# Kernel tuning notes

Hardware: AMD Instinct MI355X
Metric: run time of the kernel (lower is better)

The kernel has to match this reference:

```python
import jax, jax.numpy as jnp
import numpy as np

HEAD = 8


def setup_inputs() -> dict:
    key0 = jax.random.key(0)
    ks = jax.random.split(key0, 16)
    B, K, RD, NH = 16, 1024, 1024, 1024
    s = 0.02
    inp = {
        "v": jax.random.normal(ks[0], (B, K, RD), jnp.float32),
        "key": jax.random.normal(ks[1], (B, K, RD), jnp.float32),
        "query": jax.random.normal(ks[2], (B, K, RD), jnp.float32),
        "mask": jax.random.randint(ks[3], (B, 1, 1, K), 0, 2).astype(bool),
        # FCNet([relation_dim, num_hid], act='') == Linear(relation_dim, num_hid)
        "Wq": jax.random.normal(ks[4], (RD, NH), jnp.float32) * s,
        "bq": jnp.zeros((NH,), jnp.float32),
        "Wk": jax.random.normal(ks[5], (RD, NH), jnp.float32) * s,
        "bk": jnp.zeros((NH,), jnp.float32),
        "Wv": jax.random.normal(ks[6], (RD, NH), jnp.float32) * s,
        "bv": jnp.zeros((NH,), jnp.float32),
        "Wm": jax.random.normal(ks[7], (NH, NH), jnp.float32) * s,
        "bm": jnp.zeros((NH,), jnp.float32),
    }
    return inp


def reference(v, key, query, mask, Wq, bq, Wk, bk, Wv, bv, Wm, bm):
    B, K, _ = v.shape
    NH = Wq.shape[1]
    dk = NH // HEAD

    def split_heads(x):  # [B,K,NH] -> [B,H,K,dk]
        return x.reshape(B, K, HEAD, dk).transpose(0, 2, 1, 3)

    q = split_heads(query @ Wq + bq)
    k = split_heads(key @ Wk + bk)
    vv = split_heads(v @ Wv + bv)

    scores = jnp.einsum("bhqd,bhkd->bhqk", q, k) / jnp.sqrt(jnp.float32(dk))
    scores = jnp.where(mask, jnp.float32(-1e9), scores)
    att = jax.nn.softmax(scores, axis=-1)  # dropout is identity at eval
    atted = jnp.einsum("bhqk,bhkd->bhqd", att, vv)
    atted = atted.transpose(0, 2, 1, 3).reshape(B, K, NH)
    atted = atted @ Wm + bm
    return atted, att
```

## Files before the change

kernel.cpp:

```cpp
#include <hip/hip_runtime.h>

typedef unsigned short u16;
typedef __attribute__((ext_vector_type(8))) short short8;
typedef __attribute__((ext_vector_type(4))) float floatx4;

#define MFMA16(a, b, c) __builtin_amdgcn_mfma_f32_16x16x32_bf16(a, b, c, 0, 0, 0)

#define BB 16
#define KK 1024
#define NH 1024
#define HD 8
#define DK 128
#define ATT_OFF 16777216

typedef const __attribute__((address_space(1))) unsigned gl_u32;
typedef __attribute__((address_space(3))) unsigned lds_u32;

__device__ __forceinline__ u16 f2bf(float x) {
  unsigned u = __builtin_bit_cast(unsigned, x);
  u += 0x7fffu + ((u >> 16) & 1u);
  return (u16)(u >> 16);
}

__device__ __forceinline__ void gload16(const u16* g, u16* l) {
  __builtin_amdgcn_global_load_lds((gl_u32*)g, (lds_u32*)l, 16, 0, 0);
}

__global__ __launch_bounds__(256) void cast3_bf16x8(
    const float* __restrict__ i0, const float* __restrict__ i1,
    const float* __restrict__ i2, u16* __restrict__ o0, u16* __restrict__ o1,
    u16* __restrict__ o2) {
  const float* in = blockIdx.y == 0 ? i0 : (blockIdx.y == 1 ? i1 : i2);
  u16* out = blockIdx.y == 0 ? o0 : (blockIdx.y == 1 ? o1 : o2);
  const size_t i = ((size_t)blockIdx.x * 256 + threadIdx.x) * 8;
  float4 f0 = *(const float4*)(in + i);
  float4 f1 = *(const float4*)(in + i + 4);
  union { u16 u[8]; uint4 v; } p;
  p.u[0] = f2bf(f0.x); p.u[1] = f2bf(f0.y); p.u[2] = f2bf(f0.z); p.u[3] = f2bf(f0.w);
  p.u[4] = f2bf(f1.x); p.u[5] = f2bf(f1.y); p.u[6] = f2bf(f1.z); p.u[7] = f2bf(f1.w);
  *(uint4*)(out + i) = p.v;
}

__global__ __launch_bounds__(256) void tr_w4(
    const float* __restrict__ w0, const float* __restrict__ w1,
    const float* __restrict__ w2, const float* __restrict__ w3,
    u16* __restrict__ o0, u16* __restrict__ o1, u16* __restrict__ o2,
    u16* __restrict__ o3) {
  const int z = blockIdx.z;
  const float* in = z == 0 ? w0 : (z == 1 ? w1 : (z == 2 ? w2 : w3));
  u16* out = z == 0 ? o0 : (z == 1 ? o1 : (z == 2 ? o2 : o3));
  __shared__ u16 t[32][36];
  const int tid = threadIdx.x;
  const int bx = blockIdx.x * 32;
  const int by = blockIdx.y * 32;
  const int r = tid >> 3, c4 = (tid & 7) * 4;
  float4 f = *(const float4*)(in + (size_t)(by + r) * 1024 + bx + c4);
  t[r][c4 + 0] = f2bf(f.x);
  t[r][c4 + 1] = f2bf(f.y);
  t[r][c4 + 2] = f2bf(f.z);
  t[r][c4 + 3] = f2bf(f.w);
  __syncthreads();
  union { u16 u[4]; uint2 v; } p;
#pragma unroll
  for (int i = 0; i < 4; i++) p.u[i] = t[c4 + i][r];
  *(uint2*)(out + (size_t)(bx + r) * 1024 + by + c4) = p.v;
}

__global__ __launch_bounds__(256) void tr_head(const u16* __restrict__ vvb,
                                               u16* __restrict__ vvT) {
  __shared__ u16 t[32][36];
  const int tid = threadIdx.x;
  const int bh = blockIdx.z, b = bh >> 3, h = bh & 7;
  const int i0 = blockIdx.x * 32, d0 = blockIdx.y * 32;
  const int r = tid >> 3, c4 = (tid & 7) * 4;
  union { u16 u[4]; uint2 v; } p;
  p.v = *(const uint2*)(vvb + (size_t)(b * KK + i0 + r) * NH + h * DK + d0 + c4);
  t[r][c4 + 0] = p.u[0];
  t[r][c4 + 1] = p.u[1];
  t[r][c4 + 2] = p.u[2];
  t[r][c4 + 3] = p.u[3];
  __syncthreads();
#pragma unroll
  for (int i = 0; i < 4; i++) p.u[i] = t[c4 + i][r];
  *(uint2*)(vvT + (size_t)(bh * DK + d0 + r) * KK + i0 + c4) = p.v;
}

__device__ __forceinline__ void gemm_body(
    const u16* __restrict__ Ab, const u16* __restrict__ Bb,
    const float* __restrict__ bias, u16* __restrict__ Cb, float* __restrict__ Cf,
    const int Kd, const int ldc, const int nBase, const int mBase) {
  __shared__ __align__(16) u16 As[2][128 * 32];
  __shared__ __align__(16) u16 Bs[2][128 * 32];
  const int tid = threadIdx.x;
  const int wid = tid >> 6, lane = tid & 63;
  const int wm = (wid & 1) * 64, wn = (wid >> 1) * 64;
  const int lm = lane & 15, lq = lane >> 4;
  const int rIn = lane >> 2;
  const int sSlot = (lane & 3) * 8;

  const u16* aS0 = Ab + (size_t)(mBase + (wid * 2 + 0) * 16 + rIn) * Kd + sSlot;
  const u16* aS1 = Ab + (size_t)(mBase + (wid * 2 + 1) * 16 + rIn) * Kd + sSlot;
  const u16* bS0 = Bb + (size_t)(nBase + (wid * 2 + 0) * 16 + rIn) * Kd + sSlot;
  const u16* bS1 = Bb + (size_t)(nBase + (wid * 2 + 1) * 16 + rIn) * Kd + sSlot;

  floatx4 acc[4][4] = {};

  gload16(aS0, &As[0][(wid * 2 + 0) * 512]);
  gload16(aS1, &As[0][(wid * 2 + 1) * 512]);
  gload16(bS0, &Bs[0][(wid * 2 + 0) * 512]);
  gload16(bS1, &Bs[0][(wid * 2 + 1) * 512]);
  __syncthreads();

  int cur = 0;
  for (int k0 = 0; k0 < Kd; k0 += 32) {
    const int nxt = cur ^ 1;
    if (k0 + 32 < Kd) {
      gload16(aS0 + k0 + 32, &As[nxt][(wid * 2 + 0) * 512]);
      gload16(aS1 + k0 + 32, &As[nxt][(wid * 2 + 1) * 512]);
      gload16(bS0 + k0 + 32, &Bs[nxt][(wid * 2 + 0) * 512]);
      gload16(bS1 + k0 + 32, &Bs[nxt][(wid * 2 + 1) * 512]);
    }
    short8 af[4], bfr[4];
#pragma unroll
    for (int t = 0; t < 4; t++) {
      af[t]  = *(const short8*)&As[cur][(wm + t * 16 + lm) * 32 + lq * 8];
      bfr[t] = *(const short8*)&Bs[cur][(wn + t * 16 + lm) * 32 + lq * 8];
    }
#pragma unroll
    for (int i = 0; i < 4; i++)
#pragma unroll
      for (int j = 0; j < 4; j++)
        acc[i][j] = MFMA16(af[i], bfr[j], acc[i][j]);
    __syncthreads();
    cur = nxt;
  }

#pragma unroll
  for (int i = 0; i < 4; i++) {
    const int rowL = wm + i * 16 + lq * 4;
#pragma unroll
    for (int j = 0; j < 4; j++) {
      const int col = nBase + wn + j * 16 + lm;
      const float bval = bias ? bias[col] : 0.0f;
      const size_t base = (size_t)(mBase + rowL) * ldc + col;
#pragma unroll
      for (int r = 0; r < 4; r++) {
        const float v = acc[i][j][r] + bval;
        if (Cb) Cb[base + (size_t)r * ldc] = f2bf(v);
        if (Cf) Cf[base + (size_t)r * ldc] = v;
      }
    }
  }
}

__device__ __forceinline__ int2 swz_grid() {
  const int flat = blockIdx.x + 8 * blockIdx.y;
  const int xcd = flat & 7, idx = flat >> 3;
  const int nflat = xcd * 128 + idx;
  return make_int2((nflat & 7) * 128, (nflat >> 3) * 128);
}

__global__ __launch_bounds__(256, 2) void gemm_bt(
    const u16* __restrict__ A, const u16* __restrict__ Bt,
    const float* __restrict__ bias, u16* __restrict__ Cb, float* __restrict__ Cf) {
  int2 nm = swz_grid();
  gemm_body(A, Bt, bias, Cb, Cf, 1024, 1024, nm.x, nm.y);
}

__global__ __launch_bounds__(256, 2) void gemm_qkv(
    const u16* __restrict__ A0, const u16* __restrict__ A1,
    const u16* __restrict__ A2, const u16* __restrict__ B0,
    const u16* __restrict__ B1, const u16* __restrict__ B2,
    const float* __restrict__ b0, const float* __restrict__ b1,
    const float* __restrict__ b2, u16* __restrict__ C0, u16* __restrict__ C1,
    u16* __restrict__ C2) {
  const int z = blockIdx.z;
  const u16* A = z == 0 ? A0 : (z == 1 ? A1 : A2);
  const u16* B = z == 0 ? B0 : (z == 1 ? B1 : B2);
  const float* bias = z == 0 ? b0 : (z == 1 ? b1 : b2);
  u16* C = z == 0 ? C0 : (z == 1 ? C1 : C2);
  int2 nm = swz_grid();
  gemm_body(A, B, bias, C, nullptr, 1024, 1024, nm.x, nm.y);
}

__global__ __launch_bounds__(256, 2) void scores_softmax_pv(
    const u16* __restrict__ qb, const u16* __restrict__ kb,
    const int* __restrict__ mask, const u16* __restrict__ vvT,
    float* __restrict__ att, u16* __restrict__ atp) {
  __shared__ __align__(16) u16 p_lds[32 * 1024];
  u16* msk16 = p_lds;
  float* redM = (float*)&p_lds[1024];
  float* redS = (float*)&p_lds[1280];
  const int tid = threadIdx.x;

  const int flat = blockIdx.x + 32 * blockIdx.y;
  const int xcd = flat & 7, idx = flat >> 3;
  const int bh = xcd * 16 + (idx >> 5);
  const int rowBlk = idx & 31;

  const int b = bh >> 3, h = bh & 7;
  const int wid = tid >> 6, lane = tid & 63;
  const int lm = lane & 15, lq = lane >> 4;
  const int rowG = rowBlk * 32;

  {
    int4 m = *(const int4*)(mask + (size_t)b * KK + tid * 4);
    msk16[tid * 4 + 0] = (u16)(m.x != 0);
    msk16[tid * 4 + 1] = (u16)(m.y != 0);
    msk16[tid * 4 + 2] = (u16)(m.z != 0);
    msk16[tid * 4 + 3] = (u16)(m.w != 0);
  }

  short8 qf[2][4];
#pragma unroll
  for (int g = 0; g < 2; g++) {
    const u16* qp = qb + (size_t)(b * KK + rowG + g * 16 + lm) * NH + h * DK + lq * 8;
#pragma unroll
    for (int ks = 0; ks < 4; ks++) qf[g][ks] = *(const short8*)(qp + ks * 32);
  }

  floatx4 acc[2][16] = {};
  const u16* kpB = kb + (size_t)(b * KK + wid * 256 + lm) * NH + h * DK + lq * 8;
#pragma unroll
  for (int jt = 0; jt < 16; jt++) {
    const u16* kp = kpB + (size_t)jt * 16 * NH;
    short8 k0 = *(const short8*)(kp + 0);
    short8 k1 = *(const short8*)(kp + 32);
    short8 k2 = *(const short8*)(kp + 64);
    short8 k3 = *(const short8*)(kp + 96);
    floatx4 a0 = acc[0][jt], a1 = acc[1][jt];
    a0 = MFMA16(qf[0][0], k0, a0);
    a1 = MFMA16(qf[1][0], k0, a1);
    a0 = MFMA16(qf[0][1], k1, a0);
    a1 = MFMA16(qf[1][1], k1, a1);
    a0 = MFMA16(qf[0][2], k2, a0);
    a1 = MFMA16(qf[1][2], k2, a1);
    a0 = MFMA16(qf[0][3], k3, a0);
    a1 = MFMA16(qf[1][3], k3, a1);
    acc[0][jt] = a0;
    acc[1][jt] = a1;
  }
  __syncthreads();

  const float scale = 0.08838834764831845f;
  float mrow[2][4];
#pragma unroll
  for (int g = 0; g < 2; g++)
#pragma unroll
    for (int r = 0; r < 4; r++) mrow[g][r] = -3e38f;
#pragma unroll
  for (int jt = 0; jt < 16; jt++) {
    const int col = wid * 256 + jt * 16 + lm;
    const bool mk = msk16[col] != 0;
#pragma unroll
    for (int g = 0; g < 2; g++)
#pragma unroll
      for (int r = 0; r < 4; r++) {
        float s = mk ? -1e9f : acc[g][jt][r] * scale;
        acc[g][jt][r] = s;
        mrow[g][r] = fmaxf(mrow[g][r], s);
      }
  }
#pragma unroll
  for (int off = 1; off < 16; off <<= 1)
#pragma unroll
    for (int g = 0; g < 2; g++)
#pragma unroll
      for (int r = 0; r < 4; r++)
        mrow[g][r] = fmaxf(mrow[g][r], __shfl_xor(mrow[g][r], off));
  if (lm == 0) {
#pragma unroll
    for (int g = 0; g < 2; g++)
#pragma unroll
      for (int r = 0; r < 4; r++)
        redM[wid * 32 + g * 16 + lq * 4 + r] = mrow[g][r];
  }
  __syncthreads();
#pragma unroll
  for (int g = 0; g < 2; g++)
#pragma unroll
    for (int r = 0; r < 4; r++) {
      const int e = g * 16 + lq * 4 + r;
      mrow[g][r] = fmaxf(fmaxf(redM[0 + e], redM[32 + e]),
                         fmaxf(redM[64 + e], redM[96 + e]));
    }

  float srow[2][4] = {};
#pragma unroll
  for (int jt = 0; jt < 16; jt++)
#pragma unroll
    for (int g = 0; g < 2; g++)
#pragma unroll
      for (int r = 0; r < 4; r++) {
        float e = __expf(acc[g][jt][r] - mrow[g][r]);
        acc[g][jt][r] = e;
        srow[g][r] += e;
      }
#pragma unroll
  for (int off = 1; off < 16; off <<= 1)
#pragma unroll
    for (int g = 0; g < 2; g++)
#pragma unroll
      for (int r = 0; r < 4; r++) srow[g][r] += __shfl_xor(srow[g][r], off);
  if (lm == 0) {
#pragma unroll
    for (int g = 0; g < 2; g++)
#pragma unroll
      for (int r = 0; r < 4; r++)
        redS[wid * 32 + g * 16 + lq * 4 + r] = srow[g][r];
  }
  __syncthreads();
#pragma unroll
  for (int g = 0; g < 2; g++)
#pragma unroll
    for (int r = 0; r < 4; r++) {
      const int e = g * 16 + lq * 4 + r;
      srow[g][r] = 1.0f / (redS[0 + e] + redS[32 + e] + redS[64 + e] + redS[96 + e]);
    }
  __syncthreads();

#pragma unroll
  for (int g = 0; g < 2; g++)
#pragma unroll
    for (int r = 0; r < 4; r++) {
      const int row = g * 16 + lq * 4 + r;
#pragma unroll
      for (int jt = 0; jt < 16; jt++) {
        const int col = wid * 256 + jt * 16 + lm;
        const float p = acc[g][jt][r] * srow[g][r];
        acc[g][jt][r] = p;
        p_lds[(row * 1024 + col) ^ ((row & 7) << 3)] = f2bf(p);
      }
    }
  __syncthreads();

  floatx4 pacc[2][2] = {};
  const u16* vBase = vvT + (size_t)bh * DK * KK + (size_t)(wid * 32 + lm) * KK + lq * 8;
#pragma unroll 8
  for (int s = 0; s < 32; s++) {
    short8 v0 = *(const short8*)(vBase + s * 32);
    short8 v1 = *(const short8*)(vBase + 16 * KK + s * 32);
    short8 pf0 = *(const short8*)&p_lds[((0 + lm) * 1024 + s * 32 + lq * 8) ^ ((lm & 7) << 3)];
    short8 pf1 = *(const short8*)&p_lds[((16 + lm) * 1024 + s * 32 + lq * 8) ^ ((lm & 7) << 3)];
    pacc[0][0] = MFMA16(pf0, v0, pacc[0][0]);
    pacc[0][1] = MFMA16(pf0, v1, pacc[0][1]);
    pacc[1][0] = MFMA16(pf1, v0, pacc[1][0]);
    pacc[1][1] = MFMA16(pf1, v1, pacc[1][1]);
  }

#pragma unroll
  for (int g = 0; g < 2; g++)
#pragma unroll
    for (int r = 0; r < 4; r++) {
      const int row = rowG + g * 16 + lq * 4 + r;
      atp[(size_t)(b * KK + row) * NH + h * DK + wid * 32 + 0 + lm] = f2bf(pacc[g][0][r]);
      atp[(size_t)(b * KK + row) * NH + h * DK + wid * 32 + 16 + lm] = f2bf(pacc[g][1][r]);
    }

#pragma unroll
  for (int g = 0; g < 2; g++)
#pragma unroll
    for (int r = 0; r < 4; r++) {
      const int row = g * 16 + lq * 4 + r;
      float* attRow = att + ((size_t)bh * KK + rowG + row) * KK;
#pragma unroll
      for (int jt = 0; jt < 16; jt++) {
        const int col = wid * 256 + jt * 16 + lm;
        __builtin_nontemporal_store(acc[g][jt][r], attRow + col);
      }
    }
}

extern "C" void kernel_launch(void* const* d_in, const int* in_sizes, int n_in,
                              void* d_out, int out_size, void* d_ws, size_t ws_size,
                              hipStream_t stream) {
  const float* v     = (const float*)d_in[0];
  const float* key   = (const float*)d_in[1];
  const float* query = (const float*)d_in[2];
  const int*   mask  = (const int*)d_in[3];
  const float* Wq = (const float*)d_in[4];
  const float* bq = (const float*)d_in[5];
  const float* Wk = (const float*)d_in[6];
  const float* bk = (const float*)d_in[7];
  const float* Wv = (const float*)d_in[8];
  const float* bv = (const float*)d_in[9];
  const float* Wm = (const float*)d_in[10];
  const float* bm = (const float*)d_in[11];

  float* atted = (float*)d_out;
  float* att   = atted + (size_t)ATT_OFF;

  char* ws = (char*)d_ws;
  u16* qb   = (u16*)(ws + 0);
  u16* kb   = (u16*)(ws + 33554432ll);
  u16* vvb  = (u16*)(ws + 67108864ll);
  u16* vvT  = (u16*)(ws + 100663296ll);
  u16* atp  = (u16*)(ws + 134217728ll);
  u16* WqT  = (u16*)(ws + 167772160ll);
  u16* WkT  = (u16*)(ws + 169869312ll);
  u16* WvT  = (u16*)(ws + 171966464ll);
  u16* WmT  = (u16*)(ws + 174063616ll);

  u16* cq = (u16*)att;
  u16* ck = cq + 16777216;
  u16* cv = ck + 16777216;

  cast3_bf16x8<<<dim3(8192, 3), 256, 0, stream>>>(query, key, v, cq, ck, cv);

  tr_w4<<<dim3(32, 32, 4), 256, 0, stream>>>(Wq, Wk, Wv, Wm, WqT, WkT, WvT, WmT);

  gemm_qkv<<<dim3(8, 128, 3), 256, 0, stream>>>(cq, ck, cv, WqT, WkT, WvT,
                                                bq, bk, bv, qb, kb, vvb);

  tr_head<<<dim3(32, 4, 128), 256, 0, stream>>>(vvb, vvT);

  scores_softmax_pv<<<dim3(32, 128), 256, 0, stream>>>(qb, kb, mask, vvT, att, atp);

  gemm_bt<<<dim3(8, 128), 256, 0, stream>>>(atp, WmT, bm, nullptr, atted);
}
```

Before: 1.122 ms.

## Split attention block across eight waves and add MFMA priority hints

The fused scores/softmax/PV kernel now runs with 512 threads per block, so each wave owns 128 key columns instead of 256 and half the accumulator registers. The aim is more resident waves to hide latency on the K and V loads and the large att stores. The cross-wave max and sum reductions now combine eight partials. The PV loop splits its accumulation across two interleaved accumulators, and s_setprio hints are placed around the MFMA groups. In exchange, each wave re-reads the full Q fragment and the softmax reductions do more work.

```diff
diff --git a/kernel.cpp b/kernel.cpp
--- a/kernel.cpp
+++ b/kernel.cpp
@@ -183,14 +183,14 @@
   gemm_body(A, B, bias, C, nullptr, 1024, 1024, nm.x, nm.y);
 }
 
-__global__ __launch_bounds__(256, 2) void scores_softmax_pv(
+__global__ __launch_bounds__(512, 4) void scores_softmax_pv(
     const u16* __restrict__ qb, const u16* __restrict__ kb,
     const int* __restrict__ mask, const u16* __restrict__ vvT,
     float* __restrict__ att, u16* __restrict__ atp) {
   __shared__ __align__(16) u16 p_lds[32 * 1024];
   u16* msk16 = p_lds;
   float* redM = (float*)&p_lds[1024];
-  float* redS = (float*)&p_lds[1280];
+  float* redS = (float*)&p_lds[1536];
   const int tid = threadIdx.x;
 
   const int flat = blockIdx.x + 32 * blockIdx.y;
@@ -202,13 +202,12 @@
   const int wid = tid >> 6, lane = tid & 63;
   const int lm = lane & 15, lq = lane >> 4;
   const int rowG = rowBlk * 32;
+  const int colW = wid * 128;
 
   {
-    int4 m = *(const int4*)(mask + (size_t)b * KK + tid * 4);
-    msk16[tid * 4 + 0] = (u16)(m.x != 0);
-    msk16[tid * 4 + 1] = (u16)(m.y != 0);
-    msk16[tid * 4 + 2] = (u16)(m.z != 0);
-    msk16[tid * 4 + 3] = (u16)(m.w != 0);
+    int2 m = *(const int2*)(mask + (size_t)b * KK + tid * 2);
+    msk16[tid * 2 + 0] = (u16)(m.x != 0);
+    msk16[tid * 2 + 1] = (u16)(m.y != 0);
   }
 
   short8 qf[2][4];
@@ -219,16 +218,17 @@
     for (int ks = 0; ks < 4; ks++) qf[g][ks] = *(const short8*)(qp + ks * 32);
   }
 
-  floatx4 acc[2][16] = {};
-  const u16* kpB = kb + (size_t)(b * KK + wid * 256 + lm) * NH + h * DK + lq * 8;
-#pragma unroll
-  for (int jt = 0; jt < 16; jt++) {
+  floatx4 acc[2][8] = {};
+  const u16* kpB = kb + (size_t)(b * KK + colW + lm) * NH + h * DK + lq * 8;
+#pragma unroll
+  for (int jt = 0; jt < 8; jt++) {
     const u16* kp = kpB + (size_t)jt * 16 * NH;
     short8 k0 = *(const short8*)(kp + 0);
     short8 k1 = *(const short8*)(kp + 32);
     short8 k2 = *(const short8*)(kp + 64);
     short8 k3 = *(const short8*)(kp + 96);
     floatx4 a0 = acc[0][jt], a1 = acc[1][jt];
+    __builtin_amdgcn_s_setprio(1);
     a0 = MFMA16(qf[0][0], k0, a0);
     a1 = MFMA16(qf[1][0], k0, a1);
     a0 = MFMA16(qf[0][1], k1, a0);
@@ -237,6 +237,7 @@
     a1 = MFMA16(qf[1][2], k2, a1);
     a0 = MFMA16(qf[0][3], k3, a0);
     a1 = MFMA16(qf[1][3], k3, a1);
+    __builtin_amdgcn_s_setprio(0);
     acc[0][jt] = a0;
     acc[1][jt] = a1;
   }
@@ -249,8 +250,8 @@
 #pragma unroll
     for (int r = 0; r < 4; r++) mrow[g][r] = -3e38f;
 #pragma unroll
-  for (int jt = 0; jt < 16; jt++) {
-    const int col = wid * 256 + jt * 16 + lm;
+  for (int jt = 0; jt < 8; jt++) {
+    const int col = colW + jt * 16 + lm;
     const bool mk = msk16[col] != 0;
 #pragma unroll
     for (int g = 0; g < 2; g++)
@@ -281,13 +282,15 @@
 #pragma unroll
     for (int r = 0; r < 4; r++) {
       const int e = g * 16 + lq * 4 + r;
-      mrow[g][r] = fmaxf(fmaxf(redM[0 + e], redM[32 + e]),
-                         fmaxf(redM[64 + e], redM[96 + e]));
+      float m = redM[e];
+#pragma unroll
+      for (int w = 1; w < 8; w++) m = fmaxf(m, redM[w * 32 + e]);
+      mrow[g][r] = m;
     }
 
   float srow[2][4] = {};
 #pragma unroll
-  for (int jt = 0; jt < 16; jt++)
+  for (int jt = 0; jt < 8; jt++)
 #pragma unroll
     for (int g = 0; g < 2; g++)
 #pragma unroll
@@ -315,7 +318,10 @@
 #pragma unroll
     for (int r = 0; r < 4; r++) {
       const int e = g * 16 + lq * 4 + r;
-      srow[g][r] = 1.0f / (redS[0 + e] + redS[32 + e] + redS[64 + e] + redS[96 + e]);
+      float s = redS[e];
+#pragma unroll
+      for (int w = 1; w < 8; w++) s += redS[w * 32 + e];
+      srow[g][r] = 1.0f / s;
     }
   __syncthreads();
 
@@ -325,8 +331,8 @@
     for (int r = 0; r < 4; r++) {
       const int row = g * 16 + lq * 4 + r;
 #pragma unroll
-      for (int jt = 0; jt < 16; jt++) {
-        const int col = wid * 256 + jt * 16 + lm;
+      for (int jt = 0; jt < 8; jt++) {
+        const int col = colW + jt * 16 + lm;
         const float p = acc[g][jt][r] * srow[g][r];
         acc[g][jt][r] = p;
         p_lds[(row * 1024 + col) ^ ((row & 7) << 3)] = f2bf(p);
@@ -334,28 +340,33 @@
     }
   __syncthreads();
 
-  floatx4 pacc[2][2] = {};
-  const u16* vBase = vvT + (size_t)bh * DK * KK + (size_t)(wid * 32 + lm) * KK + lq * 8;
+  floatx4 p0a = {}, p0b = {}, p1a = {}, p1b = {};
+  const u16* vBase = vvT + (size_t)bh * DK * KK + (size_t)(wid * 16 + lm) * KK + lq * 8;
 #pragma unroll 8
   for (int s = 0; s < 32; s++) {
-    short8 v0 = *(const short8*)(vBase + s * 32);
-    short8 v1 = *(const short8*)(vBase + 16 * KK + s * 32);
+    short8 vv = *(const short8*)(vBase + s * 32);
     short8 pf0 = *(const short8*)&p_lds[((0 + lm) * 1024 + s * 32 + lq * 8) ^ ((lm & 7) << 3)];
     short8 pf1 = *(const short8*)&p_lds[((16 + lm) * 1024 + s * 32 + lq * 8) ^ ((lm & 7) << 3)];
-    pacc[0][0] = MFMA16(pf0, v0, pacc[0][0]);
-    pacc[0][1] = MFMA16(pf0, v1, pacc[0][1]);
-    pacc[1][0] = MFMA16(pf1, v0, pacc[1][0]);
-    pacc[1][1] = MFMA16(pf1, v1, pacc[1][1]);
-  }
-
-#pragma unroll
-  for (int g = 0; g < 2; g++)
-#pragma unroll
-    for (int r = 0; r < 4; r++) {
-      const int row = rowG + g * 16 + lq * 4 + r;
-      atp[(size_t)(b * KK + row) * NH + h * DK + wid * 32 + 0 + lm] = f2bf(pacc[g][0][r]);
-      atp[(size_t)(b * KK + row) * NH + h * DK + wid * 32 + 16 + lm] = f2bf(pacc[g][1][r]);
-    }
+    __builtin_amdgcn_s_setprio(1);
+    if (s & 1) {
+      p0b = MFMA16(pf0, vv, p0b);
+      p1b = MFMA16(pf1, vv, p1b);
+    } else {
+      p0a = MFMA16(pf0, vv, p0a);
+      p1a = MFMA16(pf1, vv, p1a);
+    }
+    __builtin_amdgcn_s_setprio(0);
+  }
+  floatx4 o0 = p0a + p0b;
+  floatx4 o1 = p1a + p1b;
+
+#pragma unroll
+  for (int r = 0; r < 4; r++) {
+    const int row0 = rowG + 0 + lq * 4 + r;
+    const int row1 = rowG + 16 + lq * 4 + r;
+    atp[(size_t)(b * KK + row0) * NH + h * DK + wid * 16 + lm] = f2bf(o0[r]);
+    atp[(size_t)(b * KK + row1) * NH + h * DK + wid * 16 + lm] = f2bf(o1[r]);
+  }
 
 #pragma unroll
   for (int g = 0; g < 2; g++)
@@ -364,8 +375,8 @@
       const int row = g * 16 + lq * 4 + r;
       float* attRow = att + ((size_t)bh * KK + rowG + row) * KK;
 #pragma unroll
-      for (int jt = 0; jt < 16; jt++) {
-        const int col = wid * 256 + jt * 16 + lm;
+      for (int jt = 0; jt < 8; jt++) {
+        const int col = colW + jt * 16 + lm;
         __builtin_nontemporal_store(acc[g][jt][r], attRow + col);
       }
     }
@@ -414,7 +425,7 @@
 
   tr_head<<<dim3(32, 4, 128), 256, 0, stream>>>(vvb, vvT);
 
-  scores_softmax_pv<<<dim3(32, 128), 256, 0, stream>>>(qb, kb, mask, vvT, att, atp);
+  scores_softmax_pv<<<dim3(32, 128), 512, 0, stream>>>(qb, kb, mask, vvT, att, atp);
 
   gemm_bt<<<dim3(8, 128), 256, 0, stream>>>(atp, WmT, bm, nullptr, atted);
 }
```

After: 1.160 ms. 3.3% more time.
